# Performance work log

Measured on AMD Instinct MI355X. Metric: run time of the kernel, lower is better.

Reference implementation:

```python
import jax, jax.numpy as jnp
import numpy as np


def setup_inputs() -> dict:
    key = jax.random.key(0)
    k1, k2 = jax.random.split(key)
    recon_points = jax.random.normal(k1, (4, 4096, 3), dtype=jnp.float32)
    gt_points = jax.random.normal(k2, (4, 4096, 3), dtype=jnp.float32)
    return {"recon_points": recon_points, "gt_points": gt_points}


def reference(recon_points, gt_points):
    # Pairwise squared distances: [B, N, M]
    diff = recon_points[:, :, None, :] - gt_points[:, None, :, :]  # [B,N,M,D]
    dist = jnp.sum(diff * diff, axis=3)                            # [B,N,M]
    dist_min1 = jnp.min(dist, axis=2)  # nearest gt for each recon point [B,N]
    dist_min2 = jnp.min(dist, axis=1)  # nearest recon for each gt point [B,M]
    loss = (jnp.mean(dist_min1) + jnp.mean(dist_min2)) / 2
    return loss
```

## Files before the change

### kernel.cpp

```cpp
#include <hip/hip_runtime.h>

#define CD_B 4
#define CD_N 4096
#define CD_TOTAL (CD_B * CD_N)
#define TILE 256

__global__ __launch_bounds__(256, 4) void cd_tiles(const float* __restrict__ recon,
                                                   const float* __restrict__ gt,
                                                   float* __restrict__ pm,
                                                   float* __restrict__ out) {
    const int bid = blockIdx.x;
    const int b   = bid >> 8;
    const int ti  = (bid >> 4) & 15;
    const int tj  = bid & 15;
    const int t   = threadIdx.x;
    const int w   = t >> 6;
    const int l   = t & 63;

    if (bid == 0 && t == 0) out[0] = 0.f;

    __shared__ float4 rs[TILE];
    __shared__ float4 gs[TILE];
    __shared__ float  part[4][TILE];

    {
        const float* rp = recon + ((size_t)(b * CD_N + ti * TILE) + t) * 3;
        const float* gp = gt    + ((size_t)(b * CD_N + tj * TILE) + t) * 3;
        const float rx = rp[0], ry = rp[1], rz = rp[2];
        const float gx = gp[0], gy = gp[1], gz = gp[2];
        rs[t] = make_float4(rx, ry, rz, fmaf(rz, rz, fmaf(ry, ry, rx * rx)));
        gs[t] = make_float4(gx, gy, gz, fmaf(gz, gz, fmaf(gy, gy, gx * gx)));
    }
    __syncthreads();

    const float INF = __builtin_inff();

    {
        const float4 p0 = rs[l], p1 = rs[64 + l], p2 = rs[128 + l], p3 = rs[192 + l];
        const float a0x = -2.f * p0.x, a0y = -2.f * p0.y, a0z = -2.f * p0.z;
        const float a1x = -2.f * p1.x, a1y = -2.f * p1.y, a1z = -2.f * p1.z;
        const float a2x = -2.f * p2.x, a2y = -2.f * p2.y, a2z = -2.f * p2.z;
        const float a3x = -2.f * p3.x, a3y = -2.f * p3.y, a3z = -2.f * p3.z;
        float m0 = INF, m1 = INF, m2 = INF, m3 = INF;
        const int jbase = w << 6;
        #pragma unroll 8
        for (int jj = 0; jj < 64; jj += 2) {
            const float4 g0 = gs[jbase + jj];
            const float4 g1 = gs[jbase + jj + 1];
            float d0, d1;
            d0 = fmaf(a0x, g0.x, fmaf(a0y, g0.y, fmaf(a0z, g0.z, g0.w)));
            d1 = fmaf(a0x, g1.x, fmaf(a0y, g1.y, fmaf(a0z, g1.z, g1.w)));
            m0 = fminf(fminf(d0, d1), m0);
            d0 = fmaf(a1x, g0.x, fmaf(a1y, g0.y, fmaf(a1z, g0.z, g0.w)));
            d1 = fmaf(a1x, g1.x, fmaf(a1y, g1.y, fmaf(a1z, g1.z, g1.w)));
            m1 = fminf(fminf(d0, d1), m1);
            d0 = fmaf(a2x, g0.x, fmaf(a2y, g0.y, fmaf(a2z, g0.z, g0.w)));
            d1 = fmaf(a2x, g1.x, fmaf(a2y, g1.y, fmaf(a2z, g1.z, g1.w)));
            m2 = fminf(fminf(d0, d1), m2);
            d0 = fmaf(a3x, g0.x, fmaf(a3y, g0.y, fmaf(a3z, g0.z, g0.w)));
            d1 = fmaf(a3x, g1.x, fmaf(a3y, g1.y, fmaf(a3z, g1.z, g1.w)));
            m3 = fminf(fminf(d0, d1), m3);
        }
        part[w][l]       = m0;
        part[w][64 + l]  = m1;
        part[w][128 + l] = m2;
        part[w][192 + l] = m3;
    }
    __syncthreads();
    {
        const float v = fminf(fminf(part[0][t], part[1][t]),
                              fminf(part[2][t], part[3][t]));
        const float dist = fmaxf(v + rs[t].w, 0.f);
        pm[(((b << 4) + ti) << 12) + (tj << 8) + t] = dist;
    }
    __syncthreads();

    {
        const float4 q0 = gs[l], q1 = gs[64 + l], q2 = gs[128 + l], q3 = gs[192 + l];
        const float a0x = -2.f * q0.x, a0y = -2.f * q0.y, a0z = -2.f * q0.z;
        const float a1x = -2.f * q1.x, a1y = -2.f * q1.y, a1z = -2.f * q1.z;
        const float a2x = -2.f * q2.x, a2y = -2.f * q2.y, a2z = -2.f * q2.z;
        const float a3x = -2.f * q3.x, a3y = -2.f * q3.y, a3z = -2.f * q3.z;
        float m0 = INF, m1 = INF, m2 = INF, m3 = INF;
        const int ibase = w << 6;
        #pragma unroll 8
        for (int ii = 0; ii < 64; ii += 2) {
            const float4 r0 = rs[ibase + ii];
            const float4 r1 = rs[ibase + ii + 1];
            float d0, d1;
            d0 = fmaf(a0x, r0.x, fmaf(a0y, r0.y, fmaf(a0z, r0.z, r0.w)));
            d1 = fmaf(a0x, r1.x, fmaf(a0y, r1.y, fmaf(a0z, r1.z, r1.w)));
            m0 = fminf(fminf(d0, d1), m0);
            d0 = fmaf(a1x, r0.x, fmaf(a1y, r0.y, fmaf(a1z, r0.z, r0.w)));
            d1 = fmaf(a1x, r1.x, fmaf(a1y, r1.y, fmaf(a1z, r1.z, r1.w)));
            m1 = fminf(fminf(d0, d1), m1);
            d0 = fmaf(a2x, r0.x, fmaf(a2y, r0.y, fmaf(a2z, r0.z, r0.w)));
            d1 = fmaf(a2x, r1.x, fmaf(a2y, r1.y, fmaf(a2z, r1.z, r1.w)));
            m2 = fminf(fminf(d0, d1), m2);
            d0 = fmaf(a3x, r0.x, fmaf(a3y, r0.y, fmaf(a3z, r0.z, r0.w)));
            d1 = fmaf(a3x, r1.x, fmaf(a3y, r1.y, fmaf(a3z, r1.z, r1.w)));
            m3 = fminf(fminf(d0, d1), m3);
        }
        part[w][l]       = m0;
        part[w][64 + l]  = m1;
        part[w][128 + l] = m2;
        part[w][192 + l] = m3;
    }
    __syncthreads();
    {
        const float v = fminf(fminf(part[0][t], part[1][t]),
                              fminf(part[2][t], part[3][t]));
        const float dist = fmaxf(v + gs[t].w, 0.f);
        pm[262144 + (((b << 4) + tj) << 12) + (ti << 8) + t] = dist;
    }
}

__global__ __launch_bounds__(256) void cd_gather(const float* __restrict__ pm,
                                                 float* __restrict__ out) {
    const int tid = blockIdx.x * 256 + threadIdx.x;
    const int p   = tid & 255;
    const int ot  = (tid >> 8) & 15;
    const int gb  = tid >> 12;
    const float* base = pm + ((((gb << 4) + ot) << 4) << 8) + p;

    float m = base[0];
    #pragma unroll
    for (int st = 1; st < 16; ++st) m = fminf(m, base[st << 8]);

    for (int off = 32; off; off >>= 1) m += __shfl_down(m, off);
    __shared__ float ws[4];
    const int t = threadIdx.x;
    if ((t & 63) == 0) ws[t >> 6] = m;
    __syncthreads();
    if (t == 0) {
        const float s = ws[0] + ws[1] + ws[2] + ws[3];
        atomicAdd(out, s * (0.5f / (float)CD_TOTAL));
    }
}

extern "C" void kernel_launch(void* const* d_in, const int* in_sizes, int n_in,
                              void* d_out, int out_size, void* d_ws, size_t ws_size,
                              hipStream_t stream) {
    const float* recon = (const float*)d_in[0];
    const float* gt    = (const float*)d_in[1];
    float* pm  = (float*)d_ws;
    float* out = (float*)d_out;

    cd_tiles<<<CD_B * 16 * 16, 256, 0, stream>>>(recon, gt, pm, out);
    cd_gather<<<128, 256, 0, stream>>>(pm, out);
}
```

Before: 68.60 us.

## Switch shared tiles to SoA layout and use packed float2 FMA/min

Shared-memory point tiles move from float4 AoS to separate x/y/z/norm arrays so that two consecutive points load as a float2. The inner distance loops then use 2-wide vector FMA and min builtins, which can lower to packed FP32 instructions (v_pk_fma_f32) on CDNA and roughly halve the ALU instruction count. A final scalar min folds the two lanes together. The risk is that the compiler may not emit packed min, or that the extra register pressure and changed LDS access pattern offset the gain.

```diff
diff --git a/kernel.cpp b/kernel.cpp
--- a/kernel.cpp
+++ b/kernel.cpp
@@ -4,6 +4,8 @@
 #define CD_N 4096
 #define CD_TOTAL (CD_B * CD_N)
 #define TILE 256
+
+typedef float v2f __attribute__((ext_vector_type(2)));
 
 __global__ __launch_bounds__(256, 4) void cd_tiles(const float* __restrict__ recon,
                                                    const float* __restrict__ gt,
@@ -19,98 +21,112 @@
 
     if (bid == 0 && t == 0) out[0] = 0.f;
 
-    __shared__ float4 rs[TILE];
-    __shared__ float4 gs[TILE];
-    __shared__ float  part[4][TILE];
+    __shared__ alignas(16) float rxs[TILE], rys[TILE], rzs[TILE], rns[TILE];
+    __shared__ alignas(16) float gxs[TILE], gys[TILE], gzs[TILE], gns[TILE];
+    __shared__ float part[4][TILE];
 
     {
         const float* rp = recon + ((size_t)(b * CD_N + ti * TILE) + t) * 3;
         const float* gp = gt    + ((size_t)(b * CD_N + tj * TILE) + t) * 3;
         const float rx = rp[0], ry = rp[1], rz = rp[2];
         const float gx = gp[0], gy = gp[1], gz = gp[2];
-        rs[t] = make_float4(rx, ry, rz, fmaf(rz, rz, fmaf(ry, ry, rx * rx)));
-        gs[t] = make_float4(gx, gy, gz, fmaf(gz, gz, fmaf(gy, gy, gx * gx)));
+        rxs[t] = rx; rys[t] = ry; rzs[t] = rz;
+        rns[t] = fmaf(rz, rz, fmaf(ry, ry, rx * rx));
+        gxs[t] = gx; gys[t] = gy; gzs[t] = gz;
+        gns[t] = fmaf(gz, gz, fmaf(gy, gy, gx * gx));
     }
     __syncthreads();
 
     const float INF = __builtin_inff();
 
     {
-        const float4 p0 = rs[l], p1 = rs[64 + l], p2 = rs[128 + l], p3 = rs[192 + l];
-        const float a0x = -2.f * p0.x, a0y = -2.f * p0.y, a0z = -2.f * p0.z;
-        const float a1x = -2.f * p1.x, a1y = -2.f * p1.y, a1z = -2.f * p1.z;
-        const float a2x = -2.f * p2.x, a2y = -2.f * p2.y, a2z = -2.f * p2.z;
-        const float a3x = -2.f * p3.x, a3y = -2.f * p3.y, a3z = -2.f * p3.z;
-        float m0 = INF, m1 = INF, m2 = INF, m3 = INF;
+        const v2f a0x = -2.f * rxs[l],       a0y = -2.f * rys[l],       a0z = -2.f * rzs[l];
+        const v2f a1x = -2.f * rxs[64 + l],  a1y = -2.f * rys[64 + l],  a1z = -2.f * rzs[64 + l];
+        const v2f a2x = -2.f * rxs[128 + l], a2y = -2.f * rys[128 + l], a2z = -2.f * rzs[128 + l];
+        const v2f a3x = -2.f * rxs[192 + l], a3y = -2.f * rys[192 + l], a3z = -2.f * rzs[192 + l];
+        v2f m0 = INF, m1 = INF, m2 = INF, m3 = INF;
         const int jbase = w << 6;
         #pragma unroll 8
         for (int jj = 0; jj < 64; jj += 2) {
-            const float4 g0 = gs[jbase + jj];
-            const float4 g1 = gs[jbase + jj + 1];
-            float d0, d1;
-            d0 = fmaf(a0x, g0.x, fmaf(a0y, g0.y, fmaf(a0z, g0.z, g0.w)));
-            d1 = fmaf(a0x, g1.x, fmaf(a0y, g1.y, fmaf(a0z, g1.z, g1.w)));
-            m0 = fminf(fminf(d0, d1), m0);
-            d0 = fmaf(a1x, g0.x, fmaf(a1y, g0.y, fmaf(a1z, g0.z, g0.w)));
-            d1 = fmaf(a1x, g1.x, fmaf(a1y, g1.y, fmaf(a1z, g1.z, g1.w)));
-            m1 = fminf(fminf(d0, d1), m1);
-            d0 = fmaf(a2x, g0.x, fmaf(a2y, g0.y, fmaf(a2z, g0.z, g0.w)));
-            d1 = fmaf(a2x, g1.x, fmaf(a2y, g1.y, fmaf(a2z, g1.z, g1.w)));
-            m2 = fminf(fminf(d0, d1), m2);
-            d0 = fmaf(a3x, g0.x, fmaf(a3y, g0.y, fmaf(a3z, g0.z, g0.w)));
-            d1 = fmaf(a3x, g1.x, fmaf(a3y, g1.y, fmaf(a3z, g1.z, g1.w)));
-            m3 = fminf(fminf(d0, d1), m3);
+            const int j = jbase + jj;
+            const v2f gx = *(const v2f*)&gxs[j];
+            const v2f gy = *(const v2f*)&gys[j];
+            const v2f gz = *(const v2f*)&gzs[j];
+            const v2f gn = *(const v2f*)&gns[j];
+            v2f d;
+            d = __builtin_elementwise_fma(a0z, gz, gn);
+            d = __builtin_elementwise_fma(a0y, gy, d);
+            d = __builtin_elementwise_fma(a0x, gx, d);
+            m0 = __builtin_elementwise_min(m0, d);
+            d = __builtin_elementwise_fma(a1z, gz, gn);
+            d = __builtin_elementwise_fma(a1y, gy, d);
+            d = __builtin_elementwise_fma(a1x, gx, d);
+            m1 = __builtin_elementwise_min(m1, d);
+            d = __builtin_elementwise_fma(a2z, gz, gn);
+            d = __builtin_elementwise_fma(a2y, gy, d);
+            d = __builtin_elementwise_fma(a2x, gx, d);
+            m2 = __builtin_elementwise_min(m2, d);
+            d = __builtin_elementwise_fma(a3z, gz, gn);
+            d = __builtin_elementwise_fma(a3y, gy, d);
+            d = __builtin_elementwise_fma(a3x, gx, d);
+            m3 = __builtin_elementwise_min(m3, d);
         }
-        part[w][l]       = m0;
-        part[w][64 + l]  = m1;
-        part[w][128 + l] = m2;
-        part[w][192 + l] = m3;
+        part[w][l]       = fminf(m0[0], m0[1]);
+        part[w][64 + l]  = fminf(m1[0], m1[1]);
+        part[w][128 + l] = fminf(m2[0], m2[1]);
+        part[w][192 + l] = fminf(m3[0], m3[1]);
     }
     __syncthreads();
     {
         const float v = fminf(fminf(part[0][t], part[1][t]),
                               fminf(part[2][t], part[3][t]));
-        const float dist = fmaxf(v + rs[t].w, 0.f);
+        const float dist = fmaxf(v + rns[t], 0.f);
         pm[(((b << 4) + ti) << 12) + (tj << 8) + t] = dist;
     }
     __syncthreads();
 
     {
-        const float4 q0 = gs[l], q1 = gs[64 + l], q2 = gs[128 + l], q3 = gs[192 + l];
-        const float a0x = -2.f * q0.x, a0y = -2.f * q0.y, a0z = -2.f * q0.z;
-        const float a1x = -2.f * q1.x, a1y = -2.f * q1.y, a1z = -2.f * q1.z;
-        const float a2x = -2.f * q2.x, a2y = -2.f * q2.y, a2z = -2.f * q2.z;
-        const float a3x = -2.f * q3.x, a3y = -2.f * q3.y, a3z = -2.f * q3.z;
-        float m0 = INF, m1 = INF, m2 = INF, m3 = INF;
+        const v2f a0x = -2.f * gxs[l],       a0y = -2.f * gys[l],       a0z = -2.f * gzs[l];
+        const v2f a1x = -2.f * gxs[64 + l],  a1y = -2.f * gys[64 + l],  a1z = -2.f * gzs[64 + l];
+        const v2f a2x = -2.f * gxs[128 + l], a2y = -2.f * gys[128 + l], a2z = -2.f * gzs[128 + l];
+        const v2f a3x = -2.f * gxs[192 + l], a3y = -2.f * gys[192 + l], a3z = -2.f * gzs[192 + l];
+        v2f m0 = INF, m1 = INF, m2 = INF, m3 = INF;
         const int ibase = w << 6;
         #pragma unroll 8
         for (int ii = 0; ii < 64; ii += 2) {
-            const float4 r0 = rs[ibase + ii];
-            const float4 r1 = rs[ibase + ii + 1];
-            float d0, d1;
-            d0 = fmaf(a0x, r0.x, fmaf(a0y, r0.y, fmaf(a0z, r0.z, r0.w)));
-            d1 = fmaf(a0x, r1.x, fmaf(a0y, r1.y, fmaf(a0z, r1.z, r1.w)));
-            m0 = fminf(fminf(d0, d1), m0);
-            d0 = fmaf(a1x, r0.x, fmaf(a1y, r0.y, fmaf(a1z, r0.z, r0.w)));
-            d1 = fmaf(a1x, r1.x, fmaf(a1y, r1.y, fmaf(a1z, r1.z, r1.w)));
-            m1 = fminf(fminf(d0, d1), m1);
-            d0 = fmaf(a2x, r0.x, fmaf(a2y, r0.y, fmaf(a2z, r0.z, r0.w)));
-            d1 = fmaf(a2x, r1.x, fmaf(a2y, r1.y, fmaf(a2z, r1.z, r1.w)));
-            m2 = fminf(fminf(d0, d1), m2);
-            d0 = fmaf(a3x, r0.x, fmaf(a3y, r0.y, fmaf(a3z, r0.z, r0.w)));
-            d1 = fmaf(a3x, r1.x, fmaf(a3y, r1.y, fmaf(a3z, r1.z, r1.w)));
-            m3 = fminf(fminf(d0, d1), m3);
+            const int i = ibase + ii;
+            const v2f rx = *(const v2f*)&rxs[i];
+            const v2f ry = *(const v2f*)&rys[i];
+            const v2f rz = *(const v2f*)&rzs[i];
+            const v2f rn = *(const v2f*)&rns[i];
+            v2f d;
+            d = __builtin_elementwise_fma(a0z, rz, rn);
+            d = __builtin_elementwise_fma(a0y, ry, d);
+            d = __builtin_elementwise_fma(a0x, rx, d);
+            m0 = __builtin_elementwise_min(m0, d);
+            d = __builtin_elementwise_fma(a1z, rz, rn);
+            d = __builtin_elementwise_fma(a1y, ry, d);
+            d = __builtin_elementwise_fma(a1x, rx, d);
+            m1 = __builtin_elementwise_min(m1, d);
+            d = __builtin_elementwise_fma(a2z, rz, rn);
+            d = __builtin_elementwise_fma(a2y, ry, d);
+            d = __builtin_elementwise_fma(a2x, rx, d);
+            m2 = __builtin_elementwise_min(m2, d);
+            d = __builtin_elementwise_fma(a3z, rz, rn);
+            d = __builtin_elementwise_fma(a3y, ry, d);
+            d = __builtin_elementwise_fma(a3x, rx, d);
+            m3 = __builtin_elementwise_min(m3, d);
         }
-        part[w][l]       = m0;
-        part[w][64 + l]  = m1;
-        part[w][128 + l] = m2;
-        part[w][192 + l] = m3;
+        part[w][l]       = fminf(m0[0], m0[1]);
+        part[w][64 + l]  = fminf(m1[0], m1[1]);
+        part[w][128 + l] = fminf(m2[0], m2[1]);
+        part[w][192 + l] = fminf(m3[0], m3[1]);
     }
     __syncthreads();
     {
         const float v = fminf(fminf(part[0][t], part[1][t]),
                               fminf(part[2][t], part[3][t]));
-        const float dist = fmaxf(v + gs[t].w, 0.f);
+        const float dist = fmaxf(v + gns[t], 0.f);
         pm[262144 + (((b << 4) + tj) << 12) + (ti << 8) + t] = dist;
     }
 }
```

After: 69.55 us. About the same (+1.4%).
